# Optimization experiments

Measured on AMD Instinct MI355X. Metric: run time of the kernel, lower is better.

## Reference

```python
import jax, jax.numpy as jnp
import numpy as np

L, D, H, V, S, HID = 4, 1024, 16, 32000, 2048, 2816
HD = D // H  # 64
EPS = 1e-5


def setup_inputs() -> dict:
    key = jax.random.key(0)
    ks = jax.random.split(key, 10)
    s = 0.02  # init scale for numerical sanity; math is unaffected
    return {
        "tokens": jax.random.randint(ks[0], (1, S), 0, V),
        "emb": jax.random.normal(ks[1], (V, D), jnp.float32) * s,
        "wq": jax.random.normal(ks[2], (L, D, D), jnp.float32) * s,
        "wk": jax.random.normal(ks[3], (L, D, D), jnp.float32) * s,
        "wv": jax.random.normal(ks[4], (L, D, D), jnp.float32) * s,
        "wo": jax.random.normal(ks[5], (L, D, D), jnp.float32) * s,
        "w1": jax.random.normal(ks[6], (L, HID, D), jnp.float32) * s,
        "w2": jax.random.normal(ks[7], (L, D, HID), jnp.float32) * s,
        "w3": jax.random.normal(ks[8], (L, HID, D), jnp.float32) * s,
        "attn_norm_w": jnp.ones((L, D), jnp.float32),
        "ffn_norm_w": jnp.ones((L, D), jnp.float32),
        "final_norm_w": jnp.ones((D,), jnp.float32),
    }


def _rmsnorm(x, w):
    return x * jax.lax.rsqrt(jnp.mean(x * x, axis=-1, keepdims=True) + EPS) * w


def _rope(x, cos, sin):
    # x: [B,S,H,HD]; interleaved pairs (..., -1, 2) as in apply_rotary_emb
    xr, xi = x[..., 0::2], x[..., 1::2]
    outr = xr * cos - xi * sin
    outi = xr * sin + xi * cos
    return jnp.stack([outr, outi], axis=-1).reshape(x.shape)


def reference(tokens, emb, wq, wk, wv, wo, w1, w2, w3, attn_norm_w, ffn_norm_w, final_norm_w):
    # precompute_freqs_cis(head_dim, seq)
    inv_freq = 1.0 / (10000.0 ** (jnp.arange(0, HD, 2, dtype=jnp.float32) / HD))
    fr = jnp.outer(jnp.arange(S, dtype=jnp.float32), inv_freq)  # [S, HD/2]
    cos = jnp.cos(fr)[None, :, None, :]
    sin = jnp.sin(fr)[None, :, None, :]
    mask = jnp.triu(jnp.full((S, S), -jnp.inf, jnp.float32), k=1)
    scale = 1.0 / jnp.sqrt(jnp.float32(HD))

    h = emb[tokens]  # [B,S,D] embedding lookup (dropout p=0 -> identity)
    B = h.shape[0]

    def block(h, p):
        Wq, Wk, Wv, Wo, W1, W2, W3, anw, fnw = p
        x = _rmsnorm(h, anw)
        q = (x @ Wq.T).reshape(B, S, H, HD)
        k = (x @ Wk.T).reshape(B, S, H, HD)
        v = (x @ Wv.T).reshape(B, S, H, HD)
        q = _rope(q, cos, sin)
        k = _rope(k, cos, sin)
        q, k, v = (t.transpose(0, 2, 1, 3) for t in (q, k, v))  # [B,H,S,HD]
        scores = jnp.einsum("bhqd,bhkd->bhqk", q, k) * scale + mask
        attn = jax.nn.softmax(scores, axis=-1)
        o = jnp.einsum("bhqk,bhkd->bhqd", attn, v)
        o = o.transpose(0, 2, 1, 3).reshape(B, S, D)
        h = h + o @ Wo.T
        y = _rmsnorm(h, fnw)
        ff = (jax.nn.silu(y @ W1.T) * (y @ W3.T)) @ W2.T
        return h + ff, None

    h, _ = jax.lax.scan(block, h, (wq, wk, wv, wo, w1, w2, w3, attn_norm_w, ffn_norm_w))
    h = _rmsnorm(h, final_norm_w)
    logits = h[:, -1:, :] @ emb.T  # output weight tied to tok_embeddings; last position only
    return logits
```

## Files before the change

### kernel.cpp

```cpp
#include <hip/hip_runtime.h>

#define LNUM 4
#define DIM 1024
#define NH 16
#define VOCAB 32000
#define SEQ 2048
#define HIDD 2816

typedef _Float16 f16;
typedef _Float16 h8_t __attribute__((ext_vector_type(8)));
typedef _Float16 h4_t __attribute__((ext_vector_type(4)));
typedef float f4_t __attribute__((ext_vector_type(4)));

#define MFMA(a, b, c) __builtin_amdgcn_mfma_f32_16x16x32_f16(a, b, c, 0, 0, 0)

__device__ __forceinline__ void async16(void* lds, const void* g) {
  __builtin_amdgcn_global_load_lds(
      (const __attribute__((address_space(1))) void*)g,
      (__attribute__((address_space(3))) void*)lds, 16, 0, 0);
}

template <int N>
__device__ __forceinline__ float ror16(float x) {
  int r = __builtin_amdgcn_update_dpp(0, __builtin_bit_cast(int, x),
                                      0x120 | N, 0xF, 0xF, true);
  return __builtin_bit_cast(float, r);
}
__device__ __forceinline__ float rmax16(float v) {
  v = fmaxf(v, ror16<1>(v));
  v = fmaxf(v, ror16<2>(v));
  v = fmaxf(v, ror16<4>(v));
  v = fmaxf(v, ror16<8>(v));
  return v;
}
__device__ __forceinline__ float rsum16(float v) {
  v += ror16<1>(v);
  v += ror16<2>(v);
  v += ror16<4>(v);
  v += ror16<8>(v);
  return v;
}
__device__ __forceinline__ float qswap(float x) {
  int r = __builtin_amdgcn_update_dpp(0, __builtin_bit_cast(int, x), 0xB1,
                                      0xF, 0xF, true);
  return __builtin_bit_cast(float, r);
}

__global__ __launch_bounds__(256) void cast_layer_k(
    const float* __restrict__ wq, const float* __restrict__ wk,
    const float* __restrict__ wv, const float* __restrict__ wo,
    const float* __restrict__ w1, const float* __restrict__ w3,
    const float* __restrict__ w2, f16* __restrict__ wqkv,
    f16* __restrict__ wod, f16* __restrict__ w13, f16* __restrict__ w2d) {
  const int DD4c = DIM * DIM / 4, HD4c = HIDD * DIM / 4;
  int i = blockIdx.x * 256 + threadIdx.x;
  const float* s;
  f16* d;
  int si, di;
  if (i < 3 * DD4c) {
    d = wqkv;
    di = i;
    if (i < DD4c) {
      s = wq; si = i;
    } else if (i < 2 * DD4c) {
      s = wk; si = i - DD4c;
    } else {
      s = wv; si = i - 2 * DD4c;
    }
  } else if (i < 4 * DD4c) {
    s = wo; si = i - 3 * DD4c; d = wod; di = si;
  } else if (i < 4 * DD4c + HD4c) {
    s = w1; si = i - 4 * DD4c; d = w13; di = si;
  } else if (i < 4 * DD4c + 2 * HD4c) {
    s = w3; si = i - 4 * DD4c - HD4c; d = w13; di = si + HD4c;
  } else {
    s = w2; si = i - 4 * DD4c - 2 * HD4c; d = w2d; di = si;
  }
  float4 v = ((const float4*)s)[si];
  ((h4_t*)d)[di] = (h4_t){(f16)v.x, (f16)v.y, (f16)v.z, (f16)v.w};
}

__global__ __launch_bounds__(256) void embed_k(const int* __restrict__ tok,
                                               const float* __restrict__ emb,
                                               float* __restrict__ h) {
  const int s = blockIdx.x, t = threadIdx.x;
  ((float4*)(h + (size_t)s * DIM))[t] =
      ((const float4*)(emb + (size_t)tok[s] * DIM))[t];
}

__global__ void rope_tab_k(float* __restrict__ tab) {
  int i = blockIdx.x * 256 + threadIdx.x;
  if (i >= SEQ * 32) return;
  int s = i >> 5, f = i & 31;
  float inv = powf(10000.f, -(float)f * (1.f / 32.f));
  float a = (float)s * inv;
  float sn, c;
  sincosf(a, &sn, &c);
  tab[i * 2] = c;
  tab[i * 2 + 1] = sn;
}

__global__ __launch_bounds__(256) void rmsnorm_k(const float* __restrict__ h,
                                                 const float* __restrict__ w,
                                                 f16* __restrict__ out) {
  const int s = blockIdx.x, t = threadIdx.x;
  float4 v = ((const float4*)(h + (size_t)s * DIM))[t];
  float ss = v.x * v.x + v.y * v.y + v.z * v.z + v.w * v.w;
#pragma unroll
  for (int d = 1; d < 64; d <<= 1) ss += __shfl_xor(ss, d);
  __shared__ float red[4];
  if ((t & 63) == 0) red[t >> 6] = ss;
  __syncthreads();
  float tot = red[0] + red[1] + red[2] + red[3];
  float sc = rsqrtf(tot * (1.f / (float)DIM) + 1e-5f);
  float4 wv = ((const float4*)w)[t];
  ((h4_t*)(out + (size_t)s * DIM))[t] =
      (h4_t){(f16)(v.x * sc * wv.x), (f16)(v.y * sc * wv.y),
             (f16)(v.z * sc * wv.z), (f16)(v.w * sc * wv.w)};
}

__global__ __launch_bounds__(256) void final_norm_k(const float* __restrict__ h,
                                                    const float* __restrict__ w,
                                                    float* __restrict__ hn) {
  const int t = threadIdx.x;
  float4 v = ((const float4*)(h + (size_t)(SEQ - 1) * DIM))[t];
  float ss = v.x * v.x + v.y * v.y + v.z * v.z + v.w * v.w;
#pragma unroll
  for (int d = 1; d < 64; d <<= 1) ss += __shfl_xor(ss, d);
  __shared__ float red[4];
  if ((t & 63) == 0) red[t >> 6] = ss;
  __syncthreads();
  float tot = red[0] + red[1] + red[2] + red[3];
  float sc = rsqrtf(tot * (1.f / (float)DIM) + 1e-5f);
  float4 wv = ((const float4*)w)[t];
  ((float4*)hn)[t] = make_float4(v.x * sc * wv.x, v.y * sc * wv.y,
                                 v.z * sc * wv.z, v.w * sc * wv.w);
}

__global__ __launch_bounds__(256) void logits_k(const float* __restrict__ hn,
                                                const float* __restrict__ emb,
                                                float* __restrict__ out) {
  const int v = blockIdx.x * 4 + (threadIdx.x >> 6);
  const int lane = threadIdx.x & 63;
  const float4* er = (const float4*)(emb + (size_t)v * DIM);
  const float4* hr = (const float4*)hn;
  float s = 0.f;
#pragma unroll
  for (int i = 0; i < 4; i++) {
    float4 a = er[lane + i * 64];
    float4 b = hr[lane + i * 64];
    s += a.x * b.x + a.y * b.y + a.z * b.z + a.w * b.w;
  }
#pragma unroll
  for (int d = 1; d < 64; d <<= 1) s += __shfl_xor(s, d);
  if (lane == 0) out[v] = s;
}

__global__ __launch_bounds__(256) void silu_k(const f16* __restrict__ g13,
                                              f16* __restrict__ t) {
  int c = blockIdx.x * 256 + threadIdx.x;
  int s = blockIdx.y;
  float g = (float)g13[(size_t)s * (2 * HIDD) + c];
  float u = (float)g13[(size_t)s * (2 * HIDD) + HIDD + c];
  float r = g / (1.f + __expf(-g)) * u;
  t[(size_t)s * HIDD + c] = (f16)r;
}

__global__ __launch_bounds__(256) void transpose_v(const f16* __restrict__ qkv,
                                                   f16* __restrict__ vT) {
  __shared__ f16 tile[32][34];
  int bs = blockIdx.x * 32;
  int bc = blockIdx.y * 32;
  int tx = threadIdx.x & 31, ty = threadIdx.x >> 5;
#pragma unroll
  for (int i = ty; i < 32; i += 8)
    tile[i][tx] = qkv[(size_t)(bs + i) * 3072 + 2048 + bc + tx];
  __syncthreads();
#pragma unroll
  for (int i = ty; i < 32; i += 8)
    vT[(size_t)(bc + i) * SEQ + bs + tx] = tile[tx][i];
}


template <int EPI>
__global__ __launch_bounds__(256) void gemm_bt(const f16* __restrict__ A,
                                               const f16* __restrict__ B,
                                               void* __restrict__ Cout, int M,
                                               int N, int K) {
  __shared__ __align__(16) f16 As[128 * 32];
  __shared__ __align__(16) f16 Bs[128 * 32];
  const int t = threadIdx.x;
  const int lane = t & 63;
  const int wave = t >> 6;
  const int wr = wave >> 1, wc = wave & 1;
  const int bm = blockIdx.x, bn = blockIdx.y;
  const int lr = lane & 15, lk = lane >> 4;
  const int sw = (lr >> 1) & 3;

  const int srow = t >> 2;
  const int scol = (((t & 3) ^ ((t >> 3) & 3))) * 8;
  const f16* gA = A + (size_t)(bm * 128 + srow) * K + scol;
  const f16* gB = B + (size_t)(bn * 128 + srow) * K + scol;
  f16* lA = As + t * 8;
  f16* lB = Bs + t * 8;

  f4_t acc[4][4];
#pragma unroll
  for (int m = 0; m < 4; m++)
#pragma unroll
    for (int n = 0; n < 4; n++) acc[m][n] = {0.f, 0.f, 0.f, 0.f};

  for (int k0 = 0; k0 < K; k0 += 32) {
    __syncthreads();
    async16(lA, gA + k0);
    async16(lA + 64 * 32, gA + (size_t)64 * K + k0);
    async16(lB, gB + k0);
    async16(lB + 64 * 32, gB + (size_t)64 * K + k0);
    __syncthreads();
    h8_t af[4], bfr[4];
#pragma unroll
    for (int m = 0; m < 4; m++)
      af[m] = *(const h8_t*)(As + (wr * 64 + m * 16 + lr) * 32 +
                             ((lk ^ sw) << 3));
#pragma unroll
    for (int n = 0; n < 4; n++)
      bfr[n] = *(const h8_t*)(Bs + (wc * 64 + n * 16 + lr) * 32 +
                              ((lk ^ sw) << 3));
#pragma unroll
    for (int m = 0; m < 4; m++)
#pragma unroll
      for (int n = 0; n < 4; n++) acc[m][n] = MFMA(af[m], bfr[n], acc[m][n]);
  }

  const int orow = bm * 128 + wr * 64 + lk * 4;
  const int ocol = bn * 128 + wc * 64 + lr;
#pragma unroll
  for (int m = 0; m < 4; m++)
#pragma unroll
    for (int n = 0; n < 4; n++)
#pragma unroll
      for (int j = 0; j < 4; j++) {
        int r = orow + m * 16 + j;
        int c = ocol + n * 16;
        if (EPI == 0) {
          ((f16*)Cout)[(size_t)r * N + c] = (f16)acc[m][n][j];
        } else {
          float* pC = (float*)Cout + (size_t)r * N + c;
          *pC += acc[m][n][j];
        }
      }
}

__global__ __launch_bounds__(256) void gemm_qkv(const f16* __restrict__ A,
                                                const f16* __restrict__ B,
                                                f16* __restrict__ C,
                                                const float* __restrict__ tab) {
  const int N = 3 * DIM, K = DIM;
  __shared__ __align__(16) f16 As[128 * 32];
  __shared__ __align__(16) f16 Bs[128 * 32];
  const int t = threadIdx.x;
  const int lane = t & 63;
  const int wave = t >> 6;
  const int wr = wave >> 1, wc = wave & 1;
  const int bm = blockIdx.x, bn = blockIdx.y;
  const int lr = lane & 15, lk = lane >> 4;
  const int sw = (lr >> 1) & 3;

  const int srow = t >> 2;
  const int scol = (((t & 3) ^ ((t >> 3) & 3))) * 8;
  const f16* gA = A + (size_t)(bm * 128 + srow) * K + scol;
  const f16* gB = B + (size_t)(bn * 128 + srow) * K + scol;
  f16* lA = As + t * 8;
  f16* lB = Bs + t * 8;

  f4_t acc[4][4];
#pragma unroll
  for (int m = 0; m < 4; m++)
#pragma unroll
    for (int n = 0; n < 4; n++) acc[m][n] = {0.f, 0.f, 0.f, 0.f};

  for (int k0 = 0; k0 < K; k0 += 32) {
    __syncthreads();
    async16(lA, gA + k0);
    async16(lA + 64 * 32, gA + (size_t)64 * K + k0);
    async16(lB, gB + k0);
    async16(lB + 64 * 32, gB + (size_t)64 * K + k0);
    __syncthreads();
    h8_t af[4], bfr[4];
#pragma unroll
    for (int m = 0; m < 4; m++)
      af[m] = *(const h8_t*)(As + (wr * 64 + m * 16 + lr) * 32 +
                             ((lk ^ sw) << 3));
#pragma unroll
    for (int n = 0; n < 4; n++)
      bfr[n] = *(const h8_t*)(Bs + (wc * 64 + n * 16 + lr) * 32 +
                              ((lk ^ sw) << 3));
#pragma unroll
    for (int m = 0; m < 4; m++)
#pragma unroll
      for (int n = 0; n < 4; n++) acc[m][n] = MFMA(af[m], bfr[n], acc[m][n]);
  }

  const int orow = bm * 128 + wr * 64 + lk * 4;
  const int ocol = bn * 128 + wc * 64 + lr;
  const float ssign = (lr & 1) ? 1.f : -1.f;
#pragma unroll
  for (int m = 0; m < 4; m++)
#pragma unroll
    for (int n = 0; n < 4; n++) {
      const int c = ocol + n * 16;
      const bool qk = c < 2048;
      const int f = (n * 16 + lr) >> 1;
#pragma unroll
      for (int j = 0; j < 4; j++) {
        int r = orow + m * 16 + j;
        float sv = acc[m][n][j];
        float pa = qswap(sv);
        if (qk) {
          float2 cs = ((const float2*)tab)[r * 32 + f];
          sv = sv * cs.x + pa * cs.y * ssign;
        }
        C[(size_t)r * N + c] = (f16)sv;
      }
    }
}

__global__ __launch_bounds__(256) void gemm_skp(const f16* __restrict__ A,
                                                const f16* __restrict__ B,
                                                float* __restrict__ Cp, int N,
                                                int ld, int Ks) {
  __shared__ __align__(16) f16 As[128 * 32];
  __shared__ __align__(16) f16 Bs[128 * 32];
  const int t = threadIdx.x;
  const int lane = t & 63;
  const int wave = t >> 6;
  const int wr = wave >> 1, wc = wave & 1;
  const int bm = blockIdx.x, bn = blockIdx.y, bk = blockIdx.z;
  const int lr = lane & 15, lk = lane >> 4;
  const int sw = (lr >> 1) & 3;

  const f16* Ao = A + (size_t)bk * Ks;
  const f16* Bo = B + (size_t)bk * Ks;
  float* Cout = Cp + (size_t)bk * gridDim.x * 128 * N;

  const int srow = t >> 2;
  const int scol = (((t & 3) ^ ((t >> 3) & 3))) * 8;
  const f16* gA = Ao + (size_t)(bm * 128 + srow) * ld + scol;
  const f16* gB = Bo + (size_t)(bn * 128 + srow) * ld + scol;
  f16* lA = As + t * 8;
  f16* lB = Bs + t * 8;

  f4_t acc[4][4];
#pragma unroll
  for (int m = 0; m < 4; m++)
#pragma unroll
    for (int n = 0; n < 4; n++) acc[m][n] = {0.f, 0.f, 0.f, 0.f};

  for (int k0 = 0; k0 < Ks; k0 += 32) {
    __syncthreads();
    async16(lA, gA + k0);
    async16(lA + 64 * 32, gA + (size_t)64 * ld + k0);
    async16(lB, gB + k0);
    async16(lB + 64 * 32, gB + (size_t)64 * ld + k0);
    __syncthreads();
    h8_t af[4], bfr[4];
#pragma unroll
    for (int m = 0; m < 4; m++)
      af[m] = *(const h8_t*)(As + (wr * 64 + m * 16 + lr) * 32 +
                             ((lk ^ sw) << 3));
#pragma unroll
    for (int n = 0; n < 4; n++)
      bfr[n] = *(const h8_t*)(Bs + (wc * 64 + n * 16 + lr) * 32 +
                              ((lk ^ sw) << 3));
#pragma unroll
    for (int m = 0; m < 4; m++)
#pragma unroll
      for (int n = 0; n < 4; n++) acc[m][n] = MFMA(af[m], bfr[n], acc[m][n]);
  }

  const int orow = bm * 128 + wr * 64 + lk * 4;
  const int ocol = bn * 128 + wc * 64 + lr;
#pragma unroll
  for (int m = 0; m < 4; m++)
#pragma unroll
    for (int n = 0; n < 4; n++)
#pragma unroll
      for (int j = 0; j < 4; j++)
        Cout[(size_t)(orow + m * 16 + j) * N + ocol + n * 16] = acc[m][n][j];
}

__global__ __launch_bounds__(256) void sk_reduce_k(const float* __restrict__ p,
                                                   float* __restrict__ h,
                                                   int n4) {
  int i = blockIdx.x * 256 + threadIdx.x;
  if (i >= n4) return;
  float4 a = ((const float4*)p)[i];
  float4 b = ((const float4*)p)[i + n4];
  float4 c = ((float4*)h)[i];
  c.x += a.x + b.x;
  c.y += a.y + b.y;
  c.z += a.z + b.z;
  c.w += a.w + b.w;
  ((float4*)h)[i] = c;
}

__global__ __launch_bounds__(256) void attn_k(const f16* __restrict__ qkv,
                                              const f16* __restrict__ vT,
                                              f16* __restrict__ o) {
  const int hh = blockIdx.x;
  const int qb = blockIdx.y;
  const int tid = threadIdx.x;
  const int wave = tid >> 6;
  const int lane = tid & 63;
  const int lr = lane & 15, lk = lane >> 4;
  const int q0 = qb * 32;
  __shared__ __align__(16) char P[4][4096];
  __shared__ float MBml[3][64][16];
  __shared__ f16 MBo[3][64][32];

  h8_t qf[2][2];
#pragma unroll
  for (int m = 0; m < 2; m++)
#pragma unroll
    for (int ks = 0; ks < 2; ks++)
      qf[m][ks] = *(const h8_t*)(qkv + (size_t)(q0 + m * 16 + lr) * 3072 +
                                 hh * 64 + ks * 32 + lk * 8);

  float mrow[2][4], lsum[2][4];
  f4_t oacc[2][4];
#pragma unroll
  for (int m = 0; m < 2; m++)
#pragma unroll
    for (int j = 0; j < 4; j++) {
      mrow[m][j] = -1e30f;
      lsum[m][j] = 0.f;
    }
#pragma unroll
  for (int m = 0; m < 2; m++)
#pragma unroll
    for (int n = 0; n < 4; n++) oacc[m][n] = {0.f, 0.f, 0.f, 0.f};

  const int ntiles = (qb >> 1) + 1;
  char* Pw = P[wave];
  for (int kt = wave; kt < ntiles; kt += 4) {
    f4_t sacc[2][4];
#pragma unroll
    for (int m = 0; m < 2; m++)
#pragma unroll
      for (int n = 0; n < 4; n++) sacc[m][n] = {0.f, 0.f, 0.f, 0.f};
#pragma unroll
    for (int ks = 0; ks < 2; ks++) {
      h8_t kf[4];
#pragma unroll
      for (int n = 0; n < 4; n++)
        kf[n] = *(const h8_t*)(qkv + (size_t)(kt * 64 + n * 16 + lr) * 3072 +
                               1024 + hh * 64 + ks * 32 + lk * 8);
#pragma unroll
      for (int m = 0; m < 2; m++)
#pragma unroll
        for (int n = 0; n < 4; n++)
          sacc[m][n] = MFMA(qf[m][ks], kf[n], sacc[m][n]);
    }
    const bool lastt = (kt == ntiles - 1);
    float pv[2][4][4];
#pragma unroll
    for (int m = 0; m < 2; m++)
#pragma unroll
      for (int n = 0; n < 4; n++)
#pragma unroll
        for (int j = 0; j < 4; j++) {
          float sv = sacc[m][n][j] * 0.125f;
          if (lastt && (kt * 64 + n * 16 + lr) > (q0 + m * 16 + lk * 4 + j))
            sv = -1e30f;
          pv[m][n][j] = sv;
        }
#pragma unroll
    for (int m = 0; m < 2; m++)
#pragma unroll
      for (int j = 0; j < 4; j++) {
        float mx = fmaxf(fmaxf(pv[m][0][j], pv[m][1][j]),
                         fmaxf(pv[m][2][j], pv[m][3][j]));
        mx = rmax16(mx);
        float mnew = fmaxf(mrow[m][j], mx);
        float corr = __expf(mrow[m][j] - mnew);
        mrow[m][j] = mnew;
        float rs = 0.f;
#pragma unroll
        for (int n = 0; n < 4; n++) {
          float pe = __expf(pv[m][n][j] - mnew);
          pv[m][n][j] = pe;
          rs += pe;
        }
        rs = rsum16(rs);
        lsum[m][j] = lsum[m][j] * corr + rs;
#pragma unroll
        for (int n = 0; n < 4; n++) oacc[m][n][j] *= corr;
      }
#pragma unroll
    for (int m = 0; m < 2; m++)
#pragma unroll
      for (int n = 0; n < 4; n++)
#pragma unroll
        for (int j = 0; j < 4; j++) {
          int r = m * 16 + lk * 4 + j, c = n * 16 + lr;
          int off = (r * 128 + c * 2) ^ ((r & 7) << 4);
          *(f16*)(Pw + off) = (f16)pv[m][n][j];
        }
#pragma unroll
    for (int ks = 0; ks < 2; ks++) {
      h8_t pf[2], vf[4];
#pragma unroll
      for (int m = 0; m < 2; m++) {
        int r = m * 16 + lr;
        int off = (r * 128 + ks * 64 + lk * 16) ^ ((r & 7) << 4);
        pf[m] = *(const h8_t*)(Pw + off);
      }
#pragma unroll
      for (int n = 0; n < 4; n++)
        vf[n] = *(const h8_t*)(vT + (size_t)(hh * 64 + n * 16 + lr) * SEQ +
                               kt * 64 + ks * 32 + lk * 8);
#pragma unroll
      for (int m = 0; m < 2; m++)
#pragma unroll
        for (int n = 0; n < 4; n++)
          oacc[m][n] = MFMA(pf[m], vf[n], oacc[m][n]);
    }
  }

  if (wave > 0) {
    float* dml = &MBml[wave - 1][lane][0];
    f16* doo = &MBo[wave - 1][lane][0];
#pragma unroll
    for (int m = 0; m < 2; m++)
#pragma unroll
      for (int j = 0; j < 4; j++) {
        dml[m * 4 + j] = mrow[m][j];
        dml[8 + m * 4 + j] = lsum[m][j];
      }
#pragma unroll
    for (int m = 0; m < 2; m++)
#pragma unroll
      for (int n = 0; n < 4; n++)
#pragma unroll
        for (int j = 0; j < 4; j++)
          doo[m * 16 + n * 4 + j] = (f16)oacc[m][n][j];
  }
  __syncthreads();
  if (wave == 0) {
#pragma unroll
    for (int m = 0; m < 2; m++)
#pragma unroll
      for (int j = 0; j < 4; j++) {
        float M = mrow[m][j];
#pragma unroll
        for (int w = 0; w < 3; w++) M = fmaxf(M, MBml[w][lane][m * 4 + j]);
        float sc0 = __expf(mrow[m][j] - M);
        float L = lsum[m][j] * sc0;
        float scw[3];
#pragma unroll
        for (int w = 0; w < 3; w++) {
          scw[w] = __expf(MBml[w][lane][m * 4 + j] - M);
          L += MBml[w][lane][8 + m * 4 + j] * scw[w];
        }
        float invL = 1.f / L;
#pragma unroll
        for (int n = 0; n < 4; n++) {
          float val = oacc[m][n][j] * sc0;
#pragma unroll
          for (int w = 0; w < 3; w++)
            val += (float)MBo[w][lane][m * 16 + n * 4 + j] * scw[w];
          o[(size_t)(q0 + m * 16 + lk * 4 + j) * DIM + hh * 64 + n * 16 + lr] =
              (f16)(val * invL);
        }
      }
  }
}

extern "C" void kernel_launch(void* const* d_in, const int* in_sizes, int n_in,
                              void* d_out, int out_size, void* d_ws,
                              size_t ws_size, hipStream_t stream) {
  (void)in_sizes; (void)n_in; (void)out_size; (void)ws_size;
  const int* tokens = (const int*)d_in[0];
  const float* emb = (const float*)d_in[1];
  const float* wq = (const float*)d_in[2];
  const float* wk = (const float*)d_in[3];
  const float* wv = (const float*)d_in[4];
  const float* wo = (const float*)d_in[5];
  const float* w1 = (const float*)d_in[6];
  const float* w2 = (const float*)d_in[7];
  const float* w3 = (const float*)d_in[8];
  const float* anw = (const float*)d_in[9];
  const float* fnw = (const float*)d_in[10];
  const float* finw = (const float*)d_in[11];
  float* out = (float*)d_out;

  char* p = (char*)d_ws;
  auto alloc = [&](size_t bytes) {
    char* r = p;
    p += (bytes + 255) & ~(size_t)255;
    return r;
  };
  f16* wqkv_l = (f16*)alloc((size_t)3 * DIM * DIM * 2);
  f16* wo_l = (f16*)alloc((size_t)DIM * DIM * 2);
  f16* w13_l = (f16*)alloc((size_t)2 * HIDD * DIM * 2);
  f16* w2_l = (f16*)alloc((size_t)DIM * HIDD * 2);
  float* hbuf = (float*)alloc((size_t)SEQ * DIM * 4);
  f16* x_h = (f16*)alloc((size_t)SEQ * DIM * 2);
  f16* qkv_h = (f16*)alloc((size_t)SEQ * 3 * DIM * 2);
  f16* vT_h = (f16*)alloc((size_t)DIM * SEQ * 2);
  f16* o_h = (f16*)alloc((size_t)SEQ * DIM * 2);
  f16* g13_h = (f16*)alloc((size_t)SEQ * 2 * HIDD * 2);
  f16* t_h = (f16*)alloc((size_t)SEQ * HIDD * 2);
  float* skbuf = (float*)alloc((size_t)2 * SEQ * DIM * 4);
  float* tab = (float*)alloc((size_t)SEQ * 32 * 2 * 4);
  float* hn = (float*)alloc(4096);

  embed_k<<<SEQ, 256, 0, stream>>>(tokens, emb, hbuf);
  rope_tab_k<<<(SEQ * 32 + 255) / 256, 256, 0, stream>>>(tab);

  const int CAST_BLOCKS = (4 * (DIM * DIM / 4) + 3 * (HIDD * DIM / 4)) / 256;
  const int N4 = SEQ * DIM / 4;
  for (int l = 0; l < LNUM; l++) {
    const size_t offDD = (size_t)l * DIM * DIM;
    const size_t offHD = (size_t)l * HIDD * DIM;
    cast_layer_k<<<CAST_BLOCKS, 256, 0, stream>>>(
        wq + offDD, wk + offDD, wv + offDD, wo + offDD, w1 + offHD,
        w3 + offHD, w2 + offHD, wqkv_l, wo_l, w13_l, w2_l);

    rmsnorm_k<<<SEQ, 256, 0, stream>>>(hbuf, anw + (size_t)l * DIM, x_h);
    {
      dim3 g(SEQ / 128, (3 * DIM) / 128);
      gemm_qkv<<<g, 256, 0, stream>>>(x_h, wqkv_l, qkv_h, tab);
    }
    {
      dim3 g(SEQ / 32, DIM / 32);
      transpose_v<<<g, 256, 0, stream>>>(qkv_h, vT_h);
    }
    {
      dim3 g(NH, SEQ / 32);
      attn_k<<<g, 256, 0, stream>>>(qkv_h, vT_h, o_h);
    }
    {
      dim3 g(SEQ / 128, DIM / 128, 2);
      gemm_skp<<<g, 256, 0, stream>>>(o_h, wo_l, skbuf, DIM, DIM, DIM / 2);
      sk_reduce_k<<<(N4 + 255) / 256, 256, 0, stream>>>(skbuf, hbuf, N4);
    }
    rmsnorm_k<<<SEQ, 256, 0, stream>>>(hbuf, fnw + (size_t)l * DIM, x_h);
    {
      dim3 g(SEQ / 128, (2 * HIDD) / 128);
      gemm_bt<0><<<g, 256, 0, stream>>>(x_h, w13_l, g13_h, SEQ, 2 * HIDD, DIM);
    }
    {
      dim3 g(HIDD / 256, SEQ);
      silu_k<<<g, 256, 0, stream>>>(g13_h, t_h);
    }
    {
      dim3 g(SEQ / 128, DIM / 128, 2);
      gemm_skp<<<g, 256, 0, stream>>>(t_h, w2_l, skbuf, DIM, HIDD, HIDD / 2);
      sk_reduce_k<<<(N4 + 255) / 256, 256, 0, stream>>>(skbuf, hbuf, N4);
    }
  }
  final_norm_k<<<1, 256, 0, stream>>>(hbuf, finw, hn);
  logits_k<<<VOCAB / 4, 256, 0, stream>>>(hn, emb, out);
}
```

Measured before the change: 907.9 us.

## Double-buffer LDS tiles in GEMM kernels to overlap global loads with MFMA

Replaces the single-buffered K loop in the three GEMM kernels with a two-stage ping-pong LDS pipeline. The next K-slice is issued with async global-to-LDS loads while MFMAs run on the current slice, and explicit vmcnt waits and barriers replace the two __syncthreads per iteration. The goal is to hide global memory latency behind compute. It doubles LDS use per block, which may lower occupancy, and it depends on hand-written waitcnt ordering being correct.

```diff
diff --git a/kernel.cpp b/kernel.cpp
--- a/kernel.cpp
+++ b/kernel.cpp
@@ -182,13 +182,51 @@
 }
 
 
+#define GEMM_PIPE_LOOP(KLEN, LDSTRIDE)                                       \
+  {                                                                          \
+    async16(lA, gA);                                                         \
+    async16(lA + 64 * 32, gA + (size_t)64 * (LDSTRIDE));                     \
+    async16(lB, gB);                                                         \
+    async16(lB + 64 * 32, gB + (size_t)64 * (LDSTRIDE));                     \
+    for (int k0 = 0; k0 < (KLEN); k0 += 32) {                                \
+      const int cur = (k0 >> 5) & 1;                                         \
+      if (k0 + 32 < (KLEN)) {                                                \
+        const int nxt = cur ^ 1;                                             \
+        async16(lA + nxt * 4096, gA + k0 + 32);                              \
+        async16(lA + nxt * 4096 + 64 * 32,                                   \
+                gA + (size_t)64 * (LDSTRIDE) + k0 + 32);                     \
+        async16(lB + nxt * 4096, gB + k0 + 32);                              \
+        async16(lB + nxt * 4096 + 64 * 32,                                   \
+                gB + (size_t)64 * (LDSTRIDE) + k0 + 32);                     \
+        asm volatile("s_waitcnt vmcnt(4)" ::: "memory");                     \
+      } else {                                                               \
+        asm volatile("s_waitcnt vmcnt(0)" ::: "memory");                     \
+      }                                                                      \
+      asm volatile("s_barrier" ::: "memory");                                \
+      const f16* As_c = As + cur * 4096;                                     \
+      const f16* Bs_c = Bs + cur * 4096;                                     \
+      h8_t af[4], bfr[4];                                                    \
+      _Pragma("unroll") for (int m = 0; m < 4; m++) af[m] =                  \
+          *(const h8_t*)(As_c + (wr * 64 + m * 16 + lr) * 32 +               \
+                         ((lk ^ sw) << 3));                                  \
+      _Pragma("unroll") for (int n = 0; n < 4; n++) bfr[n] =                 \
+          *(const h8_t*)(Bs_c + (wc * 64 + n * 16 + lr) * 32 +               \
+                         ((lk ^ sw) << 3));                                  \
+      _Pragma("unroll") for (int m = 0; m < 4; m++)                          \
+          _Pragma("unroll") for (int n = 0; n < 4; n++) acc[m][n] =          \
+              MFMA(af[m], bfr[n], acc[m][n]);                                \
+      asm volatile("s_waitcnt lgkmcnt(0)" ::: "memory");                     \
+      asm volatile("s_barrier" ::: "memory");                                \
+    }                                                                        \
+  }
+
 template <int EPI>
 __global__ __launch_bounds__(256) void gemm_bt(const f16* __restrict__ A,
                                                const f16* __restrict__ B,
                                                void* __restrict__ Cout, int M,
                                                int N, int K) {
-  __shared__ __align__(16) f16 As[128 * 32];
-  __shared__ __align__(16) f16 Bs[128 * 32];
+  __shared__ __align__(16) f16 As[2 * 128 * 32];
+  __shared__ __align__(16) f16 Bs[2 * 128 * 32];
   const int t = threadIdx.x;
   const int lane = t & 63;
   const int wave = t >> 6;
@@ -210,27 +248,7 @@
 #pragma unroll
     for (int n = 0; n < 4; n++) acc[m][n] = {0.f, 0.f, 0.f, 0.f};
 
-  for (int k0 = 0; k0 < K; k0 += 32) {
-    __syncthreads();
-    async16(lA, gA + k0);
-    async16(lA + 64 * 32, gA + (size_t)64 * K + k0);
-    async16(lB, gB + k0);
-    async16(lB + 64 * 32, gB + (size_t)64 * K + k0);
-    __syncthreads();
-    h8_t af[4], bfr[4];
-#pragma unroll
-    for (int m = 0; m < 4; m++)
-      af[m] = *(const h8_t*)(As + (wr * 64 + m * 16 + lr) * 32 +
-                             ((lk ^ sw) << 3));
-#pragma unroll
-    for (int n = 0; n < 4; n++)
-      bfr[n] = *(const h8_t*)(Bs + (wc * 64 + n * 16 + lr) * 32 +
-                              ((lk ^ sw) << 3));
-#pragma unroll
-    for (int m = 0; m < 4; m++)
-#pragma unroll
-      for (int n = 0; n < 4; n++) acc[m][n] = MFMA(af[m], bfr[n], acc[m][n]);
-  }
+  GEMM_PIPE_LOOP(K, K)
 
   const int orow = bm * 128 + wr * 64 + lk * 4;
   const int ocol = bn * 128 + wc * 64 + lr;
@@ -256,8 +274,8 @@
                                                 f16* __restrict__ C,
                                                 const float* __restrict__ tab) {
   const int N = 3 * DIM, K = DIM;
-  __shared__ __align__(16) f16 As[128 * 32];
-  __shared__ __align__(16) f16 Bs[128 * 32];
+  __shared__ __align__(16) f16 As[2 * 128 * 32];
+  __shared__ __align__(16) f16 Bs[2 * 128 * 32];
   const int t = threadIdx.x;
   const int lane = t & 63;
   const int wave = t >> 6;
@@ -279,27 +297,7 @@
 #pragma unroll
     for (int n = 0; n < 4; n++) acc[m][n] = {0.f, 0.f, 0.f, 0.f};
 
-  for (int k0 = 0; k0 < K; k0 += 32) {
-    __syncthreads();
-    async16(lA, gA + k0);
-    async16(lA + 64 * 32, gA + (size_t)64 * K + k0);
-    async16(lB, gB + k0);
-    async16(lB + 64 * 32, gB + (size_t)64 * K + k0);
-    __syncthreads();
-    h8_t af[4], bfr[4];
-#pragma unroll
-    for (int m = 0; m < 4; m++)
-      af[m] = *(const h8_t*)(As + (wr * 64 + m * 16 + lr) * 32 +
-                             ((lk ^ sw) << 3));
-#pragma unroll
-    for (int n = 0; n < 4; n++)
-      bfr[n] = *(const h8_t*)(Bs + (wc * 64 + n * 16 + lr) * 32 +
-                              ((lk ^ sw) << 3));
-#pragma unroll
-    for (int m = 0; m < 4; m++)
-#pragma unroll
-      for (int n = 0; n < 4; n++) acc[m][n] = MFMA(af[m], bfr[n], acc[m][n]);
-  }
+  GEMM_PIPE_LOOP(K, K)
 
   const int orow = bm * 128 + wr * 64 + lk * 4;
   const int ocol = bn * 128 + wc * 64 + lr;
@@ -329,8 +327,8 @@
                                                 const f16* __restrict__ B,
                                                 float* __restrict__ Cp, int N,
                                                 int ld, int Ks) {
-  __shared__ __align__(16) f16 As[128 * 32];
-  __shared__ __align__(16) f16 Bs[128 * 32];
+  __shared__ __align__(16) f16 As[2 * 128 * 32];
+  __shared__ __align__(16) f16 Bs[2 * 128 * 32];
   const int t = threadIdx.x;
   const int lane = t & 63;
   const int wave = t >> 6;
@@ -356,27 +354,7 @@
 #pragma unroll
     for (int n = 0; n < 4; n++) acc[m][n] = {0.f, 0.f, 0.f, 0.f};
 
-  for (int k0 = 0; k0 < Ks; k0 += 32) {
-    __syncthreads();
-    async16(lA, gA + k0);
-    async16(lA + 64 * 32, gA + (size_t)64 * ld + k0);
-    async16(lB, gB + k0);
-    async16(lB + 64 * 32, gB + (size_t)64 * ld + k0);
-    __syncthreads();
-    h8_t af[4], bfr[4];
-#pragma unroll
-    for (int m = 0; m < 4; m++)
-      af[m] = *(const h8_t*)(As + (wr * 64 + m * 16 + lr) * 32 +
-                             ((lk ^ sw) << 3));
-#pragma unroll
-    for (int n = 0; n < 4; n++)
-      bfr[n] = *(const h8_t*)(Bs + (wc * 64 + n * 16 + lr) * 32 +
-                              ((lk ^ sw) << 3));
-#pragma unroll
-    for (int m = 0; m < 4; m++)
-#pragma unroll
-      for (int n = 0; n < 4; n++) acc[m][n] = MFMA(af[m], bfr[n], acc[m][n]);
-  }
+  GEMM_PIPE_LOOP(Ks, ld)
 
   const int orow = bm * 128 + wr * 64 + lk * 4;
   const int ocol = bn * 128 + wc * 64 + lr;
```

Measured after the change: 868.2 us. -4.4%, faster.
